# Performance work log

Measured on AMD Instinct MI355X. Metric: run time of the kernel, lower is better.

The kernel has to match this reference:

```python
import jax, jax.numpy as jnp
import numpy as np

FS = 3152
NFFT = 512
NPERSEG = 512
NOVERLAP = 341
STEP = NPERSEG - NOVERLAP  # 171
F_UP = 1500
F_LOW = 1


def _a_weight_linear(freqs):
    """10**(A(f)/10) with A(0) -> 0 weight (A(0) = -inf in the torch code)."""
    f1, f2, f3, f4 = 20.6, 107.7, 737.9, 12194.0
    A1000 = -2.0
    fsq = freqs ** 2
    num = (f4 ** 2) * freqs ** 4
    den = (fsq + f1 ** 2) * jnp.sqrt(fsq + f2 ** 2) * jnp.sqrt(fsq + f3 ** 2) * (fsq + f4 ** 2)
    A = 20.0 * jnp.log10(num / den) - A1000
    return jnp.where(freqs > 0, 10.0 ** (A / 10.0), 0.0)


def setup_inputs() -> dict:
    key = jax.random.key(0)
    x = jax.random.normal(key, (64, 262144), dtype=jnp.float32)
    return {"x": x}


def reference(x):
    B, T = x.shape
    nseg = (T - NPERSEG) // STEP + 1
    # Batched unfold via gather: [B, nseg, NPERSEG]
    idx = np.arange(nseg)[:, None] * STEP + np.arange(NPERSEG)[None, :]
    # periodic Hamming window (torch.hamming_window(periodic=True))
    window = (0.54 - 0.46 * jnp.cos(2.0 * jnp.pi * jnp.arange(NPERSEG) / NPERSEG)).astype(x.dtype)
    segs = x[:, idx] * window  # [B, nseg, 512]
    spec = jnp.fft.rfft(segs, n=NFFT, axis=-1)  # [B, nseg, 257]
    win_power = jnp.sum(window ** 2)
    psd = (spec.real ** 2 + spec.imag ** 2) / (win_power * FS)
    # one-sided correction: double all bins except DC and Nyquist
    scale = jnp.ones(NFFT // 2 + 1, dtype=x.dtype).at[1:-1].set(2.0)
    pxx = (psd * scale).mean(axis=1)  # [B, 257]

    freqs = jnp.arange(NFFT // 2 + 1, dtype=jnp.float32) * (FS / NFFT)
    aw = _a_weight_linear(freqs)  # [257]

    f_res = FS / NFFT
    lo = int(np.floor(F_LOW / f_res + 1)) - 1  # = 0
    hi = int(np.floor(F_UP / f_res + 1))       # = 244
    # 10**((10*log10(pxx)+A)/10) == pxx * 10**(A/10)
    band = jnp.sum(pxx[:, lo:hi] * aw[lo:hi], axis=1)  # [B]
    level_A = 10.0 * jnp.log10(band)
    return jnp.sum(level_A) / B
```

## Files before the change

kernel.cpp:

```cpp
#include <hip/hip_runtime.h>
#include <math.h>

#ifndef M_PI
#define M_PI 3.14159265358979323846
#endif

#define T_LEN   262144
#define NBATCH  64
#define STEP    171
#define NSEG    1531
#define NPAIR   766
#define WPB     128
#define HI_BIN  244

typedef float v2f __attribute__((ext_vector_type(2)));

__device__ __forceinline__ int bitrev3(int r) {
    return ((r & 1) << 2) | (r & 2) | ((r & 4) >> 2);
}

__device__ __forceinline__ void pswap32(float& a, float& b) {
    asm volatile("v_permlane32_swap_b32 %0, %1" : "+v"(a), "+v"(b));
}
__device__ __forceinline__ void pswap16(float& a, float& b) {
    asm volatile("v_permlane16_swap_b32 %0, %1" : "+v"(a), "+v"(b));
}
template <int CTRL>
__device__ __forceinline__ float dppf(float x) {
    return __int_as_float(__builtin_amdgcn_mov_dpp(__float_as_int(x), CTRL, 0xF, 0xF, true));
}
template <int OFF>
__device__ __forceinline__ float swz(float x) {
    return __int_as_float(__builtin_amdgcn_ds_swizzle(__float_as_int(x), OFF));
}

__device__ __forceinline__ v2f cmul(v2f z, v2f w) {
    v2f t, d;
    asm("v_pk_mul_f32 %0, %1, %2 op_sel_hi:[1,0]"
        : "=v"(t) : "v"(z), "v"(w));
    asm("v_pk_fma_f32 %0, %1, %2, %3 op_sel:[1,1,0] op_sel_hi:[0,1,1] neg_lo:[1,0,0]"
        : "=v"(d) : "v"(z), "v"(w), "v"(t));
    return d;
}

#define PINV(x) asm volatile("" : "+v"(x))

__global__ __launch_bounds__(256, 4) void fft_band_k(const float* __restrict__ x,
                                                     float* __restrict__ ws) {
    const int L      = threadIdx.x & 63;
    const int waveId = (int)(blockIdx.x * 256 + threadIdx.x) >> 6;
    const int b      = waveId >> 7;
    const int winb   = waveId & (WPB - 1);

    float wv[8], wt[8];
#pragma unroll
    for (int r = 0; r < 8; ++r) {
        float n = (float)(L + 64 * r);
        wv[r] = 0.54f - 0.46f * __cosf((float)(2.0 * M_PI / 512.0) * n);
        PINV(wv[r]);
    }
#pragma unroll
    for (int p = 0; p < 8; ++p) {
        int k = 4 * ((L >> 5) & 1) + 2 * ((L >> 4) & 1) + ((p >> 2) & 1)
              + 8 * ((p & 1) + 2 * ((p >> 1) & 1) + 4 * ((L >> 3) & 1)
                     + 8 * ((L >> 2) & 1) + 16 * ((L >> 1) & 1) + 32 * (L & 1));
        int mb = (k <= 256) ? k : 512 - k;
        float wgt = 0.0f;
        if (mb >= 1 && mb < HI_BIN) {
            float f   = (float)mb * (3152.0f / 512.0f);
            float fsq = f * f;
            float num = 1.48693636e8f * fsq * fsq;
            float d1  = fsq + 424.36f;
            float d2  = fsq + 11599.29f;
            float d3  = fsq + 544496.41f;
            float d4  = fsq + 1.48693636e8f;
            float ratio = (num / (d1 * d4)) * rsqrtf(d2 * d3);
            wgt = ratio * ratio * 1.6141422e-9f;
        }
        wt[p] = wgt;
        PINV(wt[p]);
    }
    v2f M[8];
#pragma unroll
    for (int r = 1; r < 8; ++r) {
        float ang = (float)(-2.0 * M_PI / 512.0) * (float)(bitrev3(r) * L);
        float s, c; __sincosf(ang, &s, &c);
        M[r] = (v2f){c, s};
        PINV(M[r]);
    }
    float c32, s32, c16, s16;
    __sincosf((float)(-2.0 * M_PI) * (float)(L & 31) / 64.0f, &s32, &c32);
    __sincosf((float)(-2.0 * M_PI) * (float)(L & 15) / 32.0f, &s16, &c16);
    v2f W32 = (v2f){c32, s32};
    v2f W16 = (v2f){c16, s16};
    v2f W8, W4, W2, g8v, g4v, g2v, g1v;
    if (L & 8) { float s, c; __sincosf((float)(-2.0 * M_PI) * (float)(L & 7) / 16.0f, &s, &c);
                 W8 = (v2f){c, s}; g8v = (v2f){-1.0f, -1.0f}; }
    else       { W8 = (v2f){1.0f, 0.0f}; g8v = (v2f){1.0f, 1.0f}; }
    if (L & 4) { float s, c; __sincosf((float)(-2.0 * M_PI) * (float)(L & 3) / 8.0f, &s, &c);
                 W4 = (v2f){c, s}; g4v = (v2f){-1.0f, -1.0f}; }
    else       { W4 = (v2f){1.0f, 0.0f}; g4v = (v2f){1.0f, 1.0f}; }
    if (L & 2) { W2 = (L & 1) ? (v2f){0.0f, -1.0f} : (v2f){1.0f, 0.0f};
                 g2v = (v2f){-1.0f, -1.0f}; }
    else       { W2 = (v2f){1.0f, 0.0f}; g2v = (v2f){1.0f, 1.0f}; }
    g1v = (L & 1) ? (v2f){-1.0f, -1.0f} : (v2f){1.0f, 1.0f};
    PINV(W32); PINV(W16); PINV(W8); PINV(W4); PINV(W2);
    PINV(g8v); PINV(g4v); PINV(g2v); PINV(g1v);

    const float C707 = 0.70710678118654752f;
    v2f W81 = (v2f){C707, -C707};
    v2f W83 = (v2f){-C707, -C707};
    v2f WNI = (v2f){0.0f, -1.0f};
    PINV(W81); PINV(W83); PINV(WNI);

    v2f acc2 = (v2f){0.0f, 0.0f};
    const float* xb = x + (size_t)b * T_LEN;

    for (int p = winb; p < NPAIR; p += WPB) {
        const int s0 = 2 * p;
        v2f z[8];
        const float* p0 = xb + s0 * STEP + L;
        float a[8], bb[8];
#pragma unroll
        for (int r = 0; r < 8; ++r) a[r] = p0[64 * r];
        if (2 * p + 1 < NSEG) {
#pragma unroll
            for (int r = 0; r < 8; ++r) bb[r] = p0[64 * r + STEP];
        } else {
#pragma unroll
            for (int r = 0; r < 8; ++r) bb[r] = 0.0f;
        }
#pragma unroll
        for (int r = 0; r < 8; ++r) z[r] = (v2f){a[r] * wv[r], bb[r] * wv[r]};

        {
            v2f d0 = z[0] - z[4]; z[0] += z[4];
            v2f d1 = z[1] - z[5]; z[1] += z[5];
            v2f d2 = z[2] - z[6]; z[2] += z[6];
            v2f d3 = z[3] - z[7]; z[3] += z[7];
            z[4] = d0;
            z[5] = cmul(d1, W81);
            z[6] = cmul(d2, WNI);
            z[7] = cmul(d3, W83);
            v2f t;
            t = z[0] - z[2]; z[0] += z[2]; z[2] = t;
            t = z[1] - z[3]; z[1] += z[3]; z[3] = cmul(t, WNI);
            t = z[4] - z[6]; z[4] += z[6]; z[6] = t;
            t = z[5] - z[7]; z[5] += z[7]; z[7] = cmul(t, WNI);
#pragma unroll
            for (int g = 0; g < 8; g += 2) {
                t = z[g] - z[g + 1]; z[g] += z[g + 1]; z[g + 1] = t;
            }
        }

#pragma unroll
        for (int r = 1; r < 8; ++r) z[r] = cmul(z[r], M[r]);

#pragma unroll
        for (int q = 0; q < 8; q += 2) {
            float a0 = z[q].x, a1 = z[q].y, b0 = z[q + 1].x, b1 = z[q + 1].y;
            pswap32(a0, b0); pswap32(a1, b1);
            v2f A = (v2f){a0, a1}, B = (v2f){b0, b1};
            v2f s = A + B, d = A - B;
            z[q] = s; z[q + 1] = cmul(d, W32);
        }
        {
            const int qs[4] = {0, 1, 4, 5};
#pragma unroll
            for (int t2 = 0; t2 < 4; ++t2) {
                const int q = qs[t2];
                float a0 = z[q].x, a1 = z[q].y, b0 = z[q + 2].x, b1 = z[q + 2].y;
                pswap16(a0, b0); pswap16(a1, b1);
                v2f A = (v2f){a0, a1}, B = (v2f){b0, b1};
                v2f s = A + B, d = A - B;
                z[q] = s; z[q + 2] = cmul(d, W16);
            }
        }
#pragma unroll
        for (int q = 0; q < 8; ++q) {
            v2f pp = (v2f){dppf<0x128>(z[q].x), dppf<0x128>(z[q].y)};
            v2f n = g8v * z[q] + pp;
            z[q] = cmul(n, W8);
        }
#pragma unroll
        for (int q = 0; q < 8; ++q) {
            v2f pp = (v2f){swz<0x101F>(z[q].x), swz<0x101F>(z[q].y)};
            v2f n = g4v * z[q] + pp;
            z[q] = cmul(n, W4);
        }
#pragma unroll
        for (int q = 0; q < 8; ++q) {
            v2f pp = (v2f){dppf<0x4E>(z[q].x), dppf<0x4E>(z[q].y)};
            v2f n = g2v * z[q] + pp;
            z[q] = cmul(n, W2);
        }
#pragma unroll
        for (int q = 0; q < 8; ++q) {
            v2f pp = (v2f){dppf<0xB1>(z[q].x), dppf<0xB1>(z[q].y)};
            v2f n = g1v * z[q] + pp;
            v2f e = n * n;
            acc2 += (v2f){wt[q], wt[q]} * e;
        }
    }

    float acc = acc2.x + acc2.y;
#pragma unroll
    for (int off = 32; off >= 1; off >>= 1) acc += __shfl_xor(acc, off, 64);
    if (L == 0) ws[waveId] = acc;
}

__global__ void finalize_k(const float* __restrict__ ws, float* __restrict__ out) {
    __shared__ float red[256];
    int t = threadIdx.x;
    int b = t & 63, g = t >> 6;
    float s = 0.0f;
    for (int i = 0; i < 32; ++i) s += ws[b * 128 + g * 32 + i];
    red[t] = s;
    __syncthreads();
    if (t < 64) {
        float band = red[t] + red[t + 64] + red[t + 128] + red[t + 192];
        float lv = 10.0f * log10f(band);
#pragma unroll
        for (int off = 32; off >= 1; off >>= 1) lv += __shfl_xor(lv, off, 64);
        if (t == 0) out[0] = lv * (1.0f / 64.0f);
    }
}

extern "C" void kernel_launch(void* const* d_in, const int* in_sizes, int n_in,
                              void* d_out, int out_size, void* d_ws, size_t ws_size,
                              hipStream_t stream) {
    const float* x = (const float*)d_in[0];
    float* out = (float*)d_out;
    float* ws  = (float*)d_ws;
    fft_band_k<<<(NBATCH * WPB) / 4, 256, 0, stream>>>(x, ws);
    finalize_k<<<1, 256, 0, stream>>>(ws, out);
}
```

Before: 113.7 us.

## Replace last three cross-lane radix-2 stages with LDS transpose and in-register radix-8

The last three radix-2 FFT stages used ds_swizzle and DPP exchanges plus twiddle multiplies. They are replaced by a per-wave LDS write/read transpose followed by an in-register radix-8 butterfly, and the A-weight bin mapping is recomputed for the new output order. Multiplication by -i now uses a single packed multiply with a sign vector, and the window is applied with packed multiplies. This trades cross-lane shuffle latency and per-stage twiddle math for LDS traffic and 16.5KB of shared memory per block, which could affect occupancy or add bank conflicts.

```diff
diff --git a/kernel.cpp b/kernel.cpp
--- a/kernel.cpp
+++ b/kernel.cpp
@@ -29,10 +29,6 @@
 __device__ __forceinline__ float dppf(float x) {
     return __int_as_float(__builtin_amdgcn_mov_dpp(__float_as_int(x), CTRL, 0xF, 0xF, true));
 }
-template <int OFF>
-__device__ __forceinline__ float swz(float x) {
-    return __int_as_float(__builtin_amdgcn_ds_swizzle(__float_as_int(x), OFF));
-}
 
 __device__ __forceinline__ v2f cmul(v2f z, v2f w) {
     v2f t, d;
@@ -42,28 +38,42 @@
         : "=v"(d) : "v"(z), "v"(w), "v"(t));
     return d;
 }
+__device__ __forceinline__ v2f cmulNI(v2f z, v2f m) {
+    v2f d;
+    asm("v_pk_mul_f32 %0, %1, %2 op_sel:[1,0] op_sel_hi:[0,1]"
+        : "=v"(d) : "v"(z), "v"(m));
+    return d;
+}
 
 #define PINV(x) asm volatile("" : "+v"(x))
 
 __global__ __launch_bounds__(256, 4) void fft_band_k(const float* __restrict__ x,
                                                      float* __restrict__ ws) {
+    __shared__ __align__(16) char ldsc[4 * 4224];
+
     const int L      = threadIdx.x & 63;
+    const int wib    = threadIdx.x >> 6;
     const int waveId = (int)(blockIdx.x * 256 + threadIdx.x) >> 6;
     const int b      = waveId >> 7;
     const int winb   = waveId & (WPB - 1);
 
-    float wv[8], wt[8];
+    char* wptr = ldsc + wib * 4224 + 8 * L;
+    char* rptr = ldsc + wib * 4224 + 528 * (L & 7) + 8 * (L & 0x38);
+
+    v2f wvp[8];
 #pragma unroll
     for (int r = 0; r < 8; ++r) {
         float n = (float)(L + 64 * r);
-        wv[r] = 0.54f - 0.46f * __cosf((float)(2.0 * M_PI / 512.0) * n);
-        PINV(wv[r]);
-    }
+        float w = 0.54f - 0.46f * __cosf((float)(2.0 * M_PI / 512.0) * n);
+        wvp[r] = (v2f){w, w};
+        PINV(wvp[r]);
+    }
+    float wt[8];
 #pragma unroll
     for (int p = 0; p < 8; ++p) {
-        int k = 4 * ((L >> 5) & 1) + 2 * ((L >> 4) & 1) + ((p >> 2) & 1)
-              + 8 * ((p & 1) + 2 * ((p >> 1) & 1) + 4 * ((L >> 3) & 1)
-                     + 8 * ((L >> 2) & 1) + 16 * ((L >> 1) & 1) + 32 * (L & 1));
+        int k = ((L >> 2) & 1) + 2 * ((L >> 4) & 1) + 4 * ((L >> 5) & 1)
+              + 8 * (L & 1) + 16 * ((L >> 1) & 1) + 32 * ((L >> 3) & 1)
+              + 64 * bitrev3(p);
         int mb = (k <= 256) ? k : 512 - k;
         float wgt = 0.0f;
         if (mb >= 1 && mb < HI_BIN) {
@@ -93,25 +103,17 @@
     __sincosf((float)(-2.0 * M_PI) * (float)(L & 15) / 32.0f, &s16, &c16);
     v2f W32 = (v2f){c32, s32};
     v2f W16 = (v2f){c16, s16};
-    v2f W8, W4, W2, g8v, g4v, g2v, g1v;
+    v2f W8, g8v;
     if (L & 8) { float s, c; __sincosf((float)(-2.0 * M_PI) * (float)(L & 7) / 16.0f, &s, &c);
                  W8 = (v2f){c, s}; g8v = (v2f){-1.0f, -1.0f}; }
     else       { W8 = (v2f){1.0f, 0.0f}; g8v = (v2f){1.0f, 1.0f}; }
-    if (L & 4) { float s, c; __sincosf((float)(-2.0 * M_PI) * (float)(L & 3) / 8.0f, &s, &c);
-                 W4 = (v2f){c, s}; g4v = (v2f){-1.0f, -1.0f}; }
-    else       { W4 = (v2f){1.0f, 0.0f}; g4v = (v2f){1.0f, 1.0f}; }
-    if (L & 2) { W2 = (L & 1) ? (v2f){0.0f, -1.0f} : (v2f){1.0f, 0.0f};
-                 g2v = (v2f){-1.0f, -1.0f}; }
-    else       { W2 = (v2f){1.0f, 0.0f}; g2v = (v2f){1.0f, 1.0f}; }
-    g1v = (L & 1) ? (v2f){-1.0f, -1.0f} : (v2f){1.0f, 1.0f};
-    PINV(W32); PINV(W16); PINV(W8); PINV(W4); PINV(W2);
-    PINV(g8v); PINV(g4v); PINV(g2v); PINV(g1v);
+    PINV(W32); PINV(W16); PINV(W8); PINV(g8v);
 
     const float C707 = 0.70710678118654752f;
-    v2f W81 = (v2f){C707, -C707};
-    v2f W83 = (v2f){-C707, -C707};
-    v2f WNI = (v2f){0.0f, -1.0f};
-    PINV(W81); PINV(W83); PINV(WNI);
+    v2f W81  = (v2f){C707, -C707};
+    v2f W83  = (v2f){-C707, -C707};
+    v2f WNIm = (v2f){1.0f, -1.0f};
+    PINV(W81); PINV(W83); PINV(WNIm);
 
     v2f acc2 = (v2f){0.0f, 0.0f};
     const float* xb = x + (size_t)b * T_LEN;
@@ -131,7 +133,10 @@
             for (int r = 0; r < 8; ++r) bb[r] = 0.0f;
         }
 #pragma unroll
-        for (int r = 0; r < 8; ++r) z[r] = (v2f){a[r] * wv[r], bb[r] * wv[r]};
+        for (int r = 0; r < 8; ++r) {
+            v2f zin = (v2f){a[r], bb[r]};
+            z[r] = zin * wvp[r];
+        }
 
         {
             v2f d0 = z[0] - z[4]; z[0] += z[4];
@@ -140,13 +145,13 @@
             v2f d3 = z[3] - z[7]; z[3] += z[7];
             z[4] = d0;
             z[5] = cmul(d1, W81);
-            z[6] = cmul(d2, WNI);
+            z[6] = cmulNI(d2, WNIm);
             z[7] = cmul(d3, W83);
             v2f t;
             t = z[0] - z[2]; z[0] += z[2]; z[2] = t;
-            t = z[1] - z[3]; z[1] += z[3]; z[3] = cmul(t, WNI);
+            t = z[1] - z[3]; z[1] += z[3]; z[3] = cmulNI(t, WNIm);
             t = z[4] - z[6]; z[4] += z[6]; z[6] = t;
-            t = z[5] - z[7]; z[5] += z[7]; z[7] = cmul(t, WNI);
+            t = z[5] - z[7]; z[5] += z[7]; z[7] = cmulNI(t, WNIm);
 #pragma unroll
             for (int g = 0; g < 8; g += 2) {
                 t = z[g] - z[g + 1]; z[g] += z[g + 1]; z[g + 1] = t;
@@ -182,23 +187,36 @@
             v2f n = g8v * z[q] + pp;
             z[q] = cmul(n, W8);
         }
+
+#pragma unroll
+        for (int q = 0; q < 8; ++q) *(v2f*)(wptr + 528 * q) = z[q];
+        v2f y[8];
+#pragma unroll
+        for (int q = 0; q < 8; ++q) y[q] = *(const v2f*)(rptr + 8 * q);
+
+        {
+            v2f d0 = y[0] - y[4]; y[0] += y[4];
+            v2f d1 = y[1] - y[5]; y[1] += y[5];
+            v2f d2 = y[2] - y[6]; y[2] += y[6];
+            v2f d3 = y[3] - y[7]; y[3] += y[7];
+            y[4] = d0;
+            y[5] = cmul(d1, W81);
+            y[6] = cmulNI(d2, WNIm);
+            y[7] = cmul(d3, W83);
+            v2f t;
+            t = y[0] - y[2]; y[0] += y[2]; y[2] = t;
+            t = y[1] - y[3]; y[1] += y[3]; y[3] = cmulNI(t, WNIm);
+            t = y[4] - y[6]; y[4] += y[6]; y[6] = t;
+            t = y[5] - y[7]; y[5] += y[7]; y[7] = cmulNI(t, WNIm);
+#pragma unroll
+            for (int g = 0; g < 8; g += 2) {
+                t = y[g] - y[g + 1]; y[g] += y[g + 1]; y[g + 1] = t;
+            }
+        }
+
 #pragma unroll
         for (int q = 0; q < 8; ++q) {
-            v2f pp = (v2f){swz<0x101F>(z[q].x), swz<0x101F>(z[q].y)};
-            v2f n = g4v * z[q] + pp;
-            z[q] = cmul(n, W4);
-        }
-#pragma unroll
-        for (int q = 0; q < 8; ++q) {
-            v2f pp = (v2f){dppf<0x4E>(z[q].x), dppf<0x4E>(z[q].y)};
-            v2f n = g2v * z[q] + pp;
-            z[q] = cmul(n, W2);
-        }
-#pragma unroll
-        for (int q = 0; q < 8; ++q) {
-            v2f pp = (v2f){dppf<0xB1>(z[q].x), dppf<0xB1>(z[q].y)};
-            v2f n = g1v * z[q] + pp;
-            v2f e = n * n;
+            v2f e = y[q] * y[q];
             acc2 += (v2f){wt[q], wt[q]} * e;
         }
     }
```

New measurement: 106.5 us, median of 2. 6.4% less time.
